# Performance work log

Measured on AMD Instinct MI355X. Metric: run time of the kernel, lower is better.

Reference implementation:

```python
import jax, jax.numpy as jnp
import numpy as np
from jax import lax

DILATIONS = [2 ** i for i in range(9)] * 5  # 45 layers
RD, SD, QD, KF = 32, 512, 256, 33  # residual, skip, quantization channels, causal kernel
PAD = int(np.sum(DILATIONS)) + KF // 2  # 2571
L_IN = 165142  # finallen = L_IN - 2*PAD = 160000


def conv1d(x, w, b, d=1):
    # x: [N, Cin, L], w: [Cout, Cin, K] -> [N, Cout, L - d*(K-1)] (VALID)
    y = lax.conv_general_dilated(x, w, window_strides=(1,), padding='VALID',
                                 rhs_dilation=(d,),
                                 dimension_numbers=('NCH', 'OIH', 'NCH'))
    return y + b[None, :, None]


def setup_inputs() -> dict:
    key = jax.random.key(0)
    ks = jax.random.split(key, 16)
    f = lambda k, s: jax.random.normal(k, s, dtype=jnp.float32) * 0.1
    return {
        'x': jax.random.normal(ks[0], (1, 1, L_IN), dtype=jnp.float32),
        'w_causal': f(ks[1], (RD, 1, KF)), 'b_causal': f(ks[2], (RD,)),
        'w_tanh': f(ks[3], (45, RD, RD, 3)), 'b_tanh': f(ks[4], (45, RD)),
        'w_sig': f(ks[5], (45, RD, RD, 3)), 'b_sig': f(ks[6], (45, RD)),
        'w_skip': f(ks[7], (45, SD, RD, 1)), 'b_skip': f(ks[8], (45, SD)),
        'w_dense': f(ks[9], (45, RD, RD, 1)), 'b_dense': f(ks[10], (45, RD)),
        'w_post1': f(ks[11], (SD, SD, 1)), 'b_post1': f(ks[12], (SD,)),
        'w_post2': f(ks[13], (QD, SD, 1)), 'b_post2': f(ks[14], (QD,)),
    }


def reference(x, w_causal, b_causal, w_tanh, b_tanh, w_sig, b_sig,
              w_skip, b_skip, w_dense, b_dense,
              w_post1, b_post1, w_post2, b_post2):
    finallen = x.shape[-1] - 2 * PAD  # static
    x = conv1d(x, w_causal, b_causal)  # [1, RD, L-32]
    skip = jnp.zeros((1, SD, finallen), dtype=jnp.float32)
    for i, d in enumerate(DILATIONS):  # fixed 45-layer stack
        xin = x[:, :, d:-d]  # residual path, matches VALID dilated conv output length
        x1 = jnp.tanh(conv1d(x, w_tanh[i], b_tanh[i], d))
        x2 = jax.nn.sigmoid(conv1d(x, w_sig[i], b_sig[i], d))
        x = x1 * x2
        cut = (x.shape[-1] - finallen) // 2  # static
        s = conv1d(x, w_skip[i], b_skip[i])  # [1, SD, cur_len]
        skip = skip + s[:, :, cut:cut + finallen]
        x = conv1d(x, w_dense[i], b_dense[i]) + xin
    h = jax.nn.relu(conv1d(jax.nn.relu(skip), w_post1, b_post1))
    return conv1d(h, w_post2, b_post2)  # [1, QD, finallen]
```

## Files before the change

### kernel.cpp

```cpp
#include <hip/hip_runtime.h>
#include <hip/hip_bf16.h>
#include <cstdio>

typedef unsigned short ushort_t;
typedef __bf16 bf16x8 __attribute__((ext_vector_type(8)));
typedef float f32x4 __attribute__((ext_vector_type(4)));

#define FL   160000
#define L0   165110
#define NL   45
#define CH   80000

__device__ __forceinline__ float tanh_fast(float x) {
    float ax = fabsf(x);
    float e  = __expf(-2.f * ax);
    float r  = (1.f - e) / (1.f + e);
    return copysignf(r, x);
}
__device__ __forceinline__ float sigmoid_fast(float x) {
    return 1.f / (1.f + __expf(-x));
}

#define GLOAD_LDS16(gp, lp) \
    __builtin_amdgcn_global_load_lds( \
        (const __attribute__((address_space(1))) void*)(gp), \
        (__attribute__((address_space(3))) void*)(lp), 16, 0, 0)

__global__ __launch_bounds__(256) void causal_kernel(
    const float* __restrict__ x, const float* __restrict__ wc,
    const float* __restrict__ bc, float* __restrict__ y)
{
    __shared__ float ws_[33 * 32];
    __shared__ float bs_[32];
    const int tid = threadIdx.x;
    for (int idx = tid; idx < 33 * 32; idx += 256) {
        int k = idx >> 5, oc = idx & 31;
        ws_[idx] = wc[oc * 33 + k];
    }
    if (tid < 32) bs_[tid] = bc[tid];
    __syncthreads();
    const int t = blockIdx.x * 256 + tid;
    if (t >= L0) return;
    float acc[32];
#pragma unroll
    for (int oc = 0; oc < 32; ++oc) acc[oc] = bs_[oc];
    for (int k = 0; k < 33; ++k) {
        float xv = x[t + k];
        const float* wp = &ws_[k * 32];
#pragma unroll
        for (int oc = 0; oc < 32; ++oc) acc[oc] += wp[oc] * xv;
    }
    float* yr = y + (size_t)t * 32;
#pragma unroll
    for (int oc = 0; oc < 32; oc += 4)
        *(float4*)(yr + oc) = make_float4(acc[oc], acc[oc+1], acc[oc+2], acc[oc+3]);
}

__global__ __launch_bounds__(256) void prepack_frag(
    const float* __restrict__ wt, const float* __restrict__ wsg,
    const float* __restrict__ wd,
    __bf16* __restrict__ fragConv, __bf16* __restrict__ fragDense)
{
    const int idx = blockIdx.x * 256 + threadIdx.x;
    if (idx < NL * 12 * 64) {
        const int lane = idx & 63;
        const int rem  = idx >> 6;
        const int slot = rem % 12, l = rem / 12;
        const int j = slot >> 2, i = slot & 3;
        const int m = (i & 1) * 16 + (lane & 15);
        const int quad = lane >> 4;
        const float* wsrc = (i < 2) ? wt : wsg;
        __bf16 v[8];
#pragma unroll
        for (int jj = 0; jj < 8; ++jj) {
            int ic = quad * 8 + jj;
            v[jj] = (__bf16)wsrc[((size_t)(l * 32 + m) * 32 + ic) * 3 + j];
        }
        *(uint4*)(fragConv + (size_t)idx * 8) = *(const uint4*)v;
    }
    if (idx < NL * 2 * 64) {
        const int lane = idx & 63;
        const int rem  = idx >> 6;
        const int i = rem & 1, l = rem >> 1;
        const int m = i * 16 + (lane & 15);
        const int quad = lane >> 4;
        __bf16 v[8];
#pragma unroll
        for (int jj = 0; jj < 8; ++jj)
            v[jj] = (__bf16)wd[(size_t)(l * 32 + m) * 32 + quad * 8 + jj];
        *(uint4*)(fragDense + (size_t)idx * 8) = *(const uint4*)v;
    }
}

__global__ __launch_bounds__(256) void layer_mfma(
    const float* __restrict__ xin,
    float* __restrict__ xout,
    __bf16* __restrict__ xslot,
    const __bf16* __restrict__ fragConv,
    const __bf16* __restrict__ fragDense,
    const float* __restrict__ bt, const float* __restrict__ bs,
    const float* __restrict__ bd,
    int d, int Lout, int S)
{
    __shared__ __bf16 gbuf[4][32][40];
    const int tid  = threadIdx.x;
    const int wave = tid >> 6, lane = tid & 63;
    const int fm = lane & 15, quad = lane >> 4;
    const int t0 = blockIdx.x * 128 + wave * 32;

    bf16x8 Ac[3][4], Ad[2];
#pragma unroll
    for (int j = 0; j < 3; ++j)
#pragma unroll
        for (int i = 0; i < 4; ++i)
            Ac[j][i] = *(const bf16x8*)(fragConv + ((j * 4 + i) * 64 + lane) * 8);
#pragma unroll
    for (int i = 0; i < 2; ++i)
        Ad[i] = *(const bf16x8*)(fragDense + (i * 64 + lane) * 8);

    f32x4 acc[4][2];
#pragma unroll
    for (int i = 0; i < 4; ++i) {
        const float* bb = (i < 2) ? (bt + i * 16) : (bs + (i - 2) * 16);
        float4 b4 = *(const float4*)(bb + quad * 4);
        f32x4 bi; bi[0] = b4.x; bi[1] = b4.y; bi[2] = b4.z; bi[3] = b4.w;
        acc[i][0] = bi; acc[i][1] = bi;
    }

#pragma unroll
    for (int j2 = 0; j2 < 2; ++j2) {
        int tl = t0 + j2 * 16 + fm;
        if (tl > Lout - 1) tl = Lout - 1;
#pragma unroll
        for (int j = 0; j < 3; ++j) {
            const float* xp = xin + (size_t)(tl + j * d) * 32 + quad * 8;
            float4 u0 = *(const float4*)xp;
            float4 u1 = *(const float4*)(xp + 4);
            bf16x8 bf;
            bf[0] = (__bf16)u0.x; bf[1] = (__bf16)u0.y;
            bf[2] = (__bf16)u0.z; bf[3] = (__bf16)u0.w;
            bf[4] = (__bf16)u1.x; bf[5] = (__bf16)u1.y;
            bf[6] = (__bf16)u1.z; bf[7] = (__bf16)u1.w;
#pragma unroll
            for (int i = 0; i < 4; ++i)
                acc[i][j2] = __builtin_amdgcn_mfma_f32_16x16x32_bf16(
                    Ac[j][i], bf, acc[i][j2], 0, 0, 0);
        }
    }

#pragma unroll
    for (int i = 0; i < 2; ++i)
#pragma unroll
        for (int j2 = 0; j2 < 2; ++j2) {
            __bf16 pk[4];
#pragma unroll
            for (int r = 0; r < 4; ++r)
                pk[r] = (__bf16)(tanh_fast(acc[i][j2][r]) *
                                 sigmoid_fast(acc[i + 2][j2][r]));
            *(uint2*)&gbuf[wave][j2 * 16 + fm][i * 16 + quad * 4] =
                *(const uint2*)pk;
        }

    {
        const int rr = lane >> 1, hh = lane & 1;
        const int t = t0 + rr, tw = t - S;
        if (t < Lout && (unsigned)tw < FL) {
            const char* gp = (const char*)&gbuf[wave][rr][0] + hh * 32;
            uint4 v0 = *(const uint4*)gp;
            uint4 v1 = *(const uint4*)(gp + 16);
            uint4* dst = (uint4*)(xslot + (size_t)tw * 1440 + hh * 16);
            dst[0] = v0; dst[1] = v1;
        }
    }

    f32x4 dacc[2][2];
#pragma unroll
    for (int i = 0; i < 2; ++i) {
        float4 b4 = *(const float4*)(bd + i * 16 + quad * 4);
        f32x4 bi; bi[0] = b4.x; bi[1] = b4.y; bi[2] = b4.z; bi[3] = b4.w;
        dacc[i][0] = bi; dacc[i][1] = bi;
    }
#pragma unroll
    for (int j2 = 0; j2 < 2; ++j2) {
        bf16x8 gb = *(const bf16x8*)&gbuf[wave][j2 * 16 + fm][quad * 8];
#pragma unroll
        for (int i = 0; i < 2; ++i)
            dacc[i][j2] = __builtin_amdgcn_mfma_f32_16x16x32_bf16(
                Ad[i], gb, dacc[i][j2], 0, 0, 0);
    }
#pragma unroll
    for (int i = 0; i < 2; ++i)
#pragma unroll
        for (int j2 = 0; j2 < 2; ++j2) {
            const int t = t0 + j2 * 16 + fm;
            if (t < Lout) {
                const int oc = i * 16 + quad * 4;
                float4 r4 = *(const float4*)(xin + (size_t)(t + d) * 32 + oc);
                float4 o;
                o.x = dacc[i][j2][0] + r4.x;
                o.y = dacc[i][j2][1] + r4.y;
                o.z = dacc[i][j2][2] + r4.z;
                o.w = dacc[i][j2][3] + r4.w;
                *(float4*)(xout + (size_t)t * 32 + oc) = o;
            }
        }
}

template<bool TSTORE>
__global__ __launch_bounds__(256) void gemm_mfma(
    const __bf16* __restrict__ A, int lda,
    const __bf16* __restrict__ Bt, int ldb,
    void* __restrict__ Cout, int ldc,
    const float* __restrict__ bias, int K)
{
    __shared__ __bf16 As[128 * 32];
    __shared__ __bf16 Bs[128 * 32];
    const int tid  = threadIdx.x;
    const int wave = tid >> 6, lane = tid & 63;
    const int m0 = blockIdx.y * 128, n0 = blockIdx.x * 128;
    const int mbase = (wave >> 1) * 64, nbase = (wave & 1) * 64;
    const int lrow = lane >> 2, lkc = (lane & 3) * 8;
    const int fm = lane & 15, quad = lane >> 4;

    f32x4 acc[4][4] = {};

    const int g0 = wave * 2, g1 = wave * 2 + 1;
    const __bf16* Ag0 = A  + (size_t)(m0 + g0 * 16 + lrow) * lda + lkc;
    const __bf16* Ag1 = A  + (size_t)(m0 + g1 * 16 + lrow) * lda + lkc;
    const __bf16* Bg0 = Bt + (size_t)(n0 + g0 * 16 + lrow) * ldb + lkc;
    const __bf16* Bg1 = Bt + (size_t)(n0 + g1 * 16 + lrow) * ldb + lkc;
    __bf16* lA0 = As + g0 * 512;
    __bf16* lA1 = As + g1 * 512;
    __bf16* lB0 = Bs + g0 * 512;
    __bf16* lB1 = Bs + g1 * 512;

    for (int k0 = 0; k0 < K; k0 += 32) {
        GLOAD_LDS16(Ag0 + k0, lA0);
        GLOAD_LDS16(Ag1 + k0, lA1);
        GLOAD_LDS16(Bg0 + k0, lB0);
        GLOAD_LDS16(Bg1 + k0, lB1);
        __syncthreads();
        bf16x8 af[4], bfr[4];
#pragma unroll
        for (int i = 0; i < 4; ++i)
            af[i] = *(const bf16x8*)(As + (mbase + i * 16 + fm) * 32 + quad * 8);
#pragma unroll
        for (int j = 0; j < 4; ++j)
            bfr[j] = *(const bf16x8*)(Bs + (nbase + j * 16 + fm) * 32 + quad * 8);
#pragma unroll
        for (int i = 0; i < 4; ++i)
#pragma unroll
            for (int j = 0; j < 4; ++j)
                acc[i][j] = __builtin_amdgcn_mfma_f32_16x16x32_bf16(
                    af[i], bfr[j], acc[i][j], 0, 0, 0);
        __syncthreads();
    }

    if (TSTORE) {
        __bf16* O = (__bf16*)Cout;
#pragma unroll
        for (int i = 0; i < 4; ++i) {
            const int m = m0 + mbase + i * 16 + quad * 4;
            const float4 bv = *(const float4*)(bias + m);
#pragma unroll
            for (int j = 0; j < 4; ++j) {
                const int n = n0 + nbase + j * 16 + fm;
                __bf16 pk[4];
                pk[0] = (__bf16)fmaxf(acc[i][j][0] + bv.x, 0.f);
                pk[1] = (__bf16)fmaxf(acc[i][j][1] + bv.y, 0.f);
                pk[2] = (__bf16)fmaxf(acc[i][j][2] + bv.z, 0.f);
                pk[3] = (__bf16)fmaxf(acc[i][j][3] + bv.w, 0.f);
                *(uint2*)(O + (size_t)n * ldc + m) = *(const uint2*)pk;
            }
        }
    } else {
        float* O = (float*)Cout;
#pragma unroll
        for (int i = 0; i < 4; ++i) {
            const int m = m0 + mbase + i * 16 + quad * 4;
            const float4 bv = *(const float4*)(bias + m);
#pragma unroll
            for (int j = 0; j < 4; ++j) {
                const int n = n0 + nbase + j * 16 + fm;
                O[(size_t)(m + 0) * ldc + n] = acc[i][j][0] + bv.x;
                O[(size_t)(m + 1) * ldc + n] = acc[i][j][1] + bv.y;
                O[(size_t)(m + 2) * ldc + n] = acc[i][j][2] + bv.z;
                O[(size_t)(m + 3) * ldc + n] = acc[i][j][3] + bv.w;
            }
        }
    }
}

__global__ __launch_bounds__(256) void repack_kernel(
    const float* __restrict__ wskip, const float* __restrict__ bskip,
    __bf16* __restrict__ wcat, float* __restrict__ bsum)
{
    const int idx = blockIdx.x * 256 + threadIdx.x;
    if (idx < 512 * 1440) {
        int oc = idx / 1440, lic = idx % 1440;
        int l = lic >> 5, ic = lic & 31;
        wcat[idx] = (__bf16)wskip[((size_t)l * 512 + oc) * 32 + ic];
    }
    if (idx < 512) {
        float s = 0.f;
        for (int l = 0; l < NL; ++l) s += bskip[l * 512 + idx];
        bsum[idx] = s;
    }
}

__global__ __launch_bounds__(256) void repack_post(
    const float* __restrict__ w1, const float* __restrict__ w2,
    __bf16* __restrict__ wp1, __bf16* __restrict__ wp2)
{
    const int idx = blockIdx.x * 256 + threadIdx.x;
    if (idx < 512 * 512) wp1[idx] = (__bf16)w1[idx];
    if (idx < 256 * 512) wp2[idx] = (__bf16)w2[idx];
}

extern "C" void kernel_launch(void* const* d_in, const int* in_sizes, int n_in,
                              void* d_out, int out_size, void* d_ws, size_t ws_size,
                              hipStream_t stream)
{
    const float* x        = (const float*)d_in[0];
    const float* w_causal = (const float*)d_in[1];
    const float* b_causal = (const float*)d_in[2];
    const float* w_tanh   = (const float*)d_in[3];
    const float* b_tanh   = (const float*)d_in[4];
    const float* w_sig    = (const float*)d_in[5];
    const float* b_sig    = (const float*)d_in[6];
    const float* w_skip   = (const float*)d_in[7];
    const float* b_skip   = (const float*)d_in[8];
    const float* w_dense  = (const float*)d_in[9];
    const float* b_dense  = (const float*)d_in[10];
    const float* w_post1  = (const float*)d_in[11];
    const float* b_post1  = (const float*)d_in[12];
    const float* w_post2  = (const float*)d_in[13];
    const float* b_post2  = (const float*)d_in[14];
    float* out = (float*)d_out;

    char* base = (char*)d_ws;
    __bf16* XcatT  = (__bf16*)base;
    __bf16* skipTc = (__bf16*)(base + 460800000);
    __bf16* hTc    = (__bf16*)(base + 542720000);
    __bf16* wcat   = (__bf16*)(base + 624640000);
    __bf16* wp1    = (__bf16*)(base + 626114560);
    __bf16* wp2    = (__bf16*)(base + 626638848);
    float*  bsum   = (float*)(base + 626900992);
    __bf16* fragConv  = (__bf16*)(base + 626903040);
    __bf16* fragDense = (__bf16*)(base + 627456000);
    float*  xb0    = (float*)(base + 460800000);
    float*  xb1    = (float*)(base + 460800000 + 21135360);
    const size_t need = 627548160;
    if (ws_size < need) {
        fprintf(stderr, "kernel_launch: ws_size %zu < needed %zu\n", ws_size, need);
        return;
    }

    repack_kernel<<<2880, 256, 0, stream>>>(w_skip, b_skip, wcat, bsum);
    repack_post<<<1024, 256, 0, stream>>>(w_post1, w_post2, wp1, wp2);
    prepack_frag<<<(NL * 12 * 64 + 255) / 256, 256, 0, stream>>>(
        w_tanh, w_sig, w_dense, fragConv, fragDense);
    causal_kernel<<<(L0 + 255) / 256, 256, 0, stream>>>(x, w_causal, b_causal, xb0);

    int Lin = L0;
    int S   = 2555;
    float* xc = xb0;
    float* xn = xb1;
    for (int l = 0; l < NL; ++l) {
        const int d = 1 << (l % 9);
        const int Lout = Lin - 2 * d;
        S -= d;
        layer_mfma<<<(Lout + 127) / 128, 256, 0, stream>>>(
            xc, xn, XcatT + l * 32,
            fragConv + (size_t)l * 12 * 64 * 8,
            fragDense + (size_t)l * 2 * 64 * 8,
            b_tanh + l * 32, b_sig + l * 32, b_dense + l * 32,
            d, Lout, S);
        float* tmp = xc; xc = xn; xn = tmp;
        Lin = Lout;
    }

    for (int c = 0; c < 2; ++c) {
        const int c0 = c * CH;
        gemm_mfma<true><<<dim3(CH / 128, 4), 256, 0, stream>>>(
            wcat, 1440, XcatT + (size_t)c0 * 1440, 1440, skipTc, 512, bsum, 1440);
        gemm_mfma<true><<<dim3(CH / 128, 4), 256, 0, stream>>>(
            wp1, 512, skipTc, 512, hTc, 512, b_post1, 512);
        gemm_mfma<false><<<dim3(CH / 128, 2), 256, 0, stream>>>(
            wp2, 512, hTc, 512, out + c0, FL, b_post2, 512);
    }
}
```

Baseline: 1.938 ms.

## Rewrite post GEMMs with 256x256 tiles, 4-stage LDS pipeline and XCD-aware remap

```diff
diff --git a/kernel.cpp b/kernel.cpp
--- a/kernel.cpp
+++ b/kernel.cpp
@@ -207,85 +207,130 @@
 }
 
 template<bool TSTORE>
-__global__ __launch_bounds__(256) void gemm_mfma(
+__global__ __launch_bounds__(512, 2) void gemm256(
     const __bf16* __restrict__ A, int lda,
     const __bf16* __restrict__ Bt, int ldb,
     void* __restrict__ Cout, int ldc,
-    const float* __restrict__ bias, int K)
-{
-    __shared__ __bf16 As[128 * 32];
-    __shared__ __bf16 Bs[128 * 32];
+    const float* __restrict__ bias, int K, int Ncur, int mTile)
+{
+    __shared__ __bf16 lds[4 * 16384];
     const int tid  = threadIdx.x;
     const int wave = tid >> 6, lane = tid & 63;
-    const int m0 = blockIdx.y * 128, n0 = blockIdx.x * 128;
-    const int mbase = (wave >> 1) * 64, nbase = (wave & 1) * 64;
-    const int lrow = lane >> 2, lkc = (lane & 3) * 8;
     const int fm = lane & 15, quad = lane >> 4;
-
-    f32x4 acc[4][4] = {};
-
-    const int g0 = wave * 2, g1 = wave * 2 + 1;
-    const __bf16* Ag0 = A  + (size_t)(m0 + g0 * 16 + lrow) * lda + lkc;
-    const __bf16* Ag1 = A  + (size_t)(m0 + g1 * 16 + lrow) * lda + lkc;
-    const __bf16* Bg0 = Bt + (size_t)(n0 + g0 * 16 + lrow) * ldb + lkc;
-    const __bf16* Bg1 = Bt + (size_t)(n0 + g1 * 16 + lrow) * ldb + lkc;
-    __bf16* lA0 = As + g0 * 512;
-    __bf16* lA1 = As + g1 * 512;
-    __bf16* lB0 = Bs + g0 * 512;
-    __bf16* lB1 = Bs + g1 * 512;
-
-    for (int k0 = 0; k0 < K; k0 += 32) {
-        GLOAD_LDS16(Ag0 + k0, lA0);
-        GLOAD_LDS16(Ag1 + k0, lA1);
-        GLOAD_LDS16(Bg0 + k0, lB0);
-        GLOAD_LDS16(Bg1 + k0, lB1);
-        __syncthreads();
-        bf16x8 af[4], bfr[4];
+    const int wm = wave >> 2, wn = wave & 3;
+
+    const int nwg = gridDim.x;
+    const int q8 = nwg >> 3, r8 = nwg & 7;
+    const int xcd = blockIdx.x & 7, loc = blockIdx.x >> 3;
+    const int sbid = (xcd < r8 ? xcd * (q8 + 1)
+                               : r8 * (q8 + 1) + (xcd - r8) * q8) + loc;
+    const int m0 = (sbid % mTile) * 256;
+    const int n0 = (sbid / mTile) * 256;
+
+    const __bf16* pS[4];
+    int dstE[4];
+#pragma unroll
+    for (int i = 0; i < 4; ++i) {
+        const int cidx = (i & 1) * 512 + tid;
+        const int r = cidx >> 2, c = cidx & 3;
+        const int cs = c ^ ((r >> 1) & 3);
+        if (i < 2) {
+            pS[i] = A + (size_t)(m0 + r) * lda + cs * 8;
+        } else {
+            int rg = n0 + r; if (rg > Ncur - 1) rg = Ncur - 1;
+            pS[i] = Bt + (size_t)rg * ldb + cs * 8;
+        }
+        dstE[i] = ((i < 2) ? 0 : 8192) + (i & 1) * 4096 + wave * 512;
+    }
+
+    const int swz = ((quad ^ ((fm >> 1) & 3)) << 3);
+    const int aoff = (wm * 128 + fm) * 32 + swz;
+    const int boff = 8192 + (wn * 64 + fm) * 32 + swz;
+
+    f32x4 acc[8][4] = {};
+
+    auto do_stage = [&](int t) {
+        const int pb = (t & 3) * 16384;
+        const int ko = t * 32;
 #pragma unroll
         for (int i = 0; i < 4; ++i)
-            af[i] = *(const bf16x8*)(As + (mbase + i * 16 + fm) * 32 + quad * 8);
+            GLOAD_LDS16(pS[i] + ko, lds + pb + dstE[i]);
+    };
+    auto tile_compute = [&](int t) {
+        const int pb = (t & 3) * 16384;
+        bf16x8 af[8], bg[4];
+#pragma unroll
+        for (int i = 0; i < 8; ++i)
+            af[i] = *(const bf16x8*)(lds + pb + aoff + i * 512);
 #pragma unroll
         for (int j = 0; j < 4; ++j)
-            bfr[j] = *(const bf16x8*)(Bs + (nbase + j * 16 + fm) * 32 + quad * 8);
-#pragma unroll
-        for (int i = 0; i < 4; ++i)
+            bg[j] = *(const bf16x8*)(lds + pb + boff + j * 512);
+        __builtin_amdgcn_s_setprio(1);
+#pragma unroll
+        for (int i = 0; i < 8; ++i)
 #pragma unroll
             for (int j = 0; j < 4; ++j)
                 acc[i][j] = __builtin_amdgcn_mfma_f32_16x16x32_bf16(
-                    af[i], bfr[j], acc[i][j], 0, 0, 0);
-        __syncthreads();
-    }
+                    af[i], bg[j], acc[i][j], 0, 0, 0);
+        __builtin_amdgcn_s_setprio(0);
+    };
+
+    const int NT = K >> 5;
+    do_stage(0); do_stage(1); do_stage(2);
+    for (int t = 0; t < NT - 3; ++t) {
+        asm volatile("s_waitcnt vmcnt(8)" ::: "memory");
+        __builtin_amdgcn_s_barrier();
+        __builtin_amdgcn_sched_barrier(0);
+        do_stage(t + 3);
+        tile_compute(t);
+    }
+    asm volatile("s_waitcnt vmcnt(8)" ::: "memory");
+    __builtin_amdgcn_s_barrier();
+    __builtin_amdgcn_sched_barrier(0);
+    tile_compute(NT - 3);
+    asm volatile("s_waitcnt vmcnt(4)" ::: "memory");
+    __builtin_amdgcn_s_barrier();
+    __builtin_amdgcn_sched_barrier(0);
+    tile_compute(NT - 2);
+    asm volatile("s_waitcnt vmcnt(0)" ::: "memory");
+    __builtin_amdgcn_s_barrier();
+    __builtin_amdgcn_sched_barrier(0);
+    tile_compute(NT - 1);
 
     if (TSTORE) {
         __bf16* O = (__bf16*)Cout;
 #pragma unroll
-        for (int i = 0; i < 4; ++i) {
-            const int m = m0 + mbase + i * 16 + quad * 4;
+        for (int i = 0; i < 8; ++i) {
+            const int m = m0 + wm * 128 + i * 16 + quad * 4;
             const float4 bv = *(const float4*)(bias + m);
 #pragma unroll
             for (int j = 0; j < 4; ++j) {
-                const int n = n0 + nbase + j * 16 + fm;
-                __bf16 pk[4];
-                pk[0] = (__bf16)fmaxf(acc[i][j][0] + bv.x, 0.f);
-                pk[1] = (__bf16)fmaxf(acc[i][j][1] + bv.y, 0.f);
-                pk[2] = (__bf16)fmaxf(acc[i][j][2] + bv.z, 0.f);
-                pk[3] = (__bf16)fmaxf(acc[i][j][3] + bv.w, 0.f);
-                *(uint2*)(O + (size_t)n * ldc + m) = *(const uint2*)pk;
+                const int n = n0 + wn * 64 + j * 16 + fm;
+                if (n < Ncur) {
+                    __bf16 pk[4];
+                    pk[0] = (__bf16)fmaxf(acc[i][j][0] + bv.x, 0.f);
+                    pk[1] = (__bf16)fmaxf(acc[i][j][1] + bv.y, 0.f);
+                    pk[2] = (__bf16)fmaxf(acc[i][j][2] + bv.z, 0.f);
+                    pk[3] = (__bf16)fmaxf(acc[i][j][3] + bv.w, 0.f);
+                    *(uint2*)(O + (size_t)n * ldc + m) = *(const uint2*)pk;
+                }
             }
         }
     } else {
         float* O = (float*)Cout;
 #pragma unroll
-        for (int i = 0; i < 4; ++i) {
-            const int m = m0 + mbase + i * 16 + quad * 4;
+        for (int i = 0; i < 8; ++i) {
+            const int m = m0 + wm * 128 + i * 16 + quad * 4;
             const float4 bv = *(const float4*)(bias + m);
 #pragma unroll
             for (int j = 0; j < 4; ++j) {
-                const int n = n0 + nbase + j * 16 + fm;
-                O[(size_t)(m + 0) * ldc + n] = acc[i][j][0] + bv.x;
-                O[(size_t)(m + 1) * ldc + n] = acc[i][j][1] + bv.y;
-                O[(size_t)(m + 2) * ldc + n] = acc[i][j][2] + bv.z;
-                O[(size_t)(m + 3) * ldc + n] = acc[i][j][3] + bv.w;
+                const int n = n0 + wn * 64 + j * 16 + fm;
+                if (n < Ncur) {
+                    O[(size_t)(m + 0) * ldc + n] = acc[i][j][0] + bv.x;
+                    O[(size_t)(m + 1) * ldc + n] = acc[i][j][1] + bv.y;
+                    O[(size_t)(m + 2) * ldc + n] = acc[i][j][2] + bv.z;
+                    O[(size_t)(m + 3) * ldc + n] = acc[i][j][3] + bv.w;
+                }
             }
         }
     }
@@ -380,13 +425,15 @@
         Lin = Lout;
     }
 
+    const int nTile = (CH + 255) / 256;
     for (int c = 0; c < 2; ++c) {
         const int c0 = c * CH;
-        gemm_mfma<true><<<dim3(CH / 128, 4), 256, 0, stream>>>(
-            wcat, 1440, XcatT + (size_t)c0 * 1440, 1440, skipTc, 512, bsum, 1440);
-        gemm_mfma<true><<<dim3(CH / 128, 4), 256, 0, stream>>>(
-            wp1, 512, skipTc, 512, hTc, 512, b_post1, 512);
-        gemm_mfma<false><<<dim3(CH / 128, 2), 256, 0, stream>>>(
-            wp2, 512, hTc, 512, out + c0, FL, b_post2, 512);
-    }
-}
+        gemm256<true><<<nTile * 2, 512, 0, stream>>>(
+            wcat, 1440, XcatT + (size_t)c0 * 1440, 1440,
+            skipTc, 512, bsum, 1440, CH, 2);
+        gemm256<true><<<nTile * 2, 512, 0, stream>>>(
+            wp1, 512, skipTc, 512, hTc, 512, b_post1, 512, CH, 2);
+        gemm256<false><<<nTile, 512, 0, stream>>>(
+            wp2, 512, hTc, 512, out + c0, FL, b_post2, 512, CH, 1);
+    }
+}
```

Result: faster. 1.780 ms (-8.2%).
